# Optimization experiments

Measured on AMD Instinct MI355X. Metric: run time of the kernel, lower is better.

## Reference

```python
import jax, jax.numpy as jnp
import numpy as np

EMBED_DIM = 1024
NUM_HEADS = 16
HEAD_DIM = EMBED_DIM // NUM_HEADS
B, T = 4, 2048


def setup_inputs() -> dict:
    key = jax.random.key(0)
    ks = jax.random.split(key, 5)
    s = 1.0 / np.sqrt(EMBED_DIM)
    x = jax.random.normal(ks[0], (B, T, EMBED_DIM), dtype=jnp.float32)
    attention_mask = jnp.ones((B, 1, 1, T), dtype=jnp.int32)
    # torch Linear weights: qkv (3E, E), out (E, E); store transposed for x @ W
    W_qkv = jax.random.uniform(ks[1], (EMBED_DIM, 3 * EMBED_DIM), jnp.float32, -s, s)
    b_qkv = jax.random.uniform(ks[2], (3 * EMBED_DIM,), jnp.float32, -s, s)
    W_out = jax.random.uniform(ks[3], (EMBED_DIM, EMBED_DIM), jnp.float32, -s, s)
    b_out = jax.random.uniform(ks[4], (EMBED_DIM,), jnp.float32, -s, s)
    return {"x": x, "attention_mask": attention_mask,
            "W_qkv": W_qkv, "b_qkv": b_qkv, "W_out": W_out, "b_out": b_out}


def reference(x, attention_mask, W_qkv, b_qkv, W_out, b_out):
    Bq, Tq, E = x.shape
    qkv = x @ W_qkv + b_qkv                              # [B,T,3E]
    qkv = qkv.reshape(Bq, Tq, 3, NUM_HEADS, HEAD_DIM)
    qkv = jnp.transpose(qkv, (2, 0, 3, 1, 4))            # [3,B,H,T,d]
    q, k, v = qkv[0], qkv[1], qkv[2]
    scores = jnp.einsum('bhqd,bhkd->bhqk', q, k) / jnp.sqrt(
        jnp.asarray(HEAD_DIM, x.dtype))                  # [B,H,T,T]
    scores = jnp.where(attention_mask == 0, jnp.asarray(-jnp.inf, x.dtype), scores)
    attn = jax.nn.softmax(scores, axis=-1)
    ctx = jnp.einsum('bhqk,bhkd->bhqd', attn, v)         # [B,H,T,d]
    ctx = jnp.transpose(ctx, (0, 2, 1, 3)).reshape(Bq, Tq, E)
    return ctx @ W_out + b_out
```

## Files before the change

kernel.cpp:

```cpp
#include <hip/hip_runtime.h>
#include <hip/hip_bf16.h>
#include <stdint.h>


typedef __attribute__((ext_vector_type(8))) short short8;
typedef __attribute__((ext_vector_type(4))) float f32x4;
typedef __attribute__((ext_vector_type(16))) float f32x16;
typedef __attribute__((ext_vector_type(4))) unsigned short ushort4_t;
typedef __attribute__((ext_vector_type(8))) unsigned short ushort8_t;

#define SEQ 2048
#define EDIM 1024
#define QSCALE 0.18033688011112042f

__device__ __forceinline__ unsigned short f2bf(float x) {
  union { float f; uint32_t u; } v; v.f = x;
  uint32_t r = v.u + 0x7fffu + ((v.u >> 16) & 1u);
  return (unsigned short)(r >> 16);
}

__device__ __forceinline__ uint32_t cvtpk(float lo, float hi) {
  uint32_t r;
  asm("v_cvt_pk_bf16_f32 %0, %1, %2" : "=v"(r) : "v"(lo), "v"(hi));
  return r;
}

__device__ __forceinline__ float exp2_raw(float x) {
  float r;
  asm("v_exp_f32 %0, %1" : "=v"(r) : "v"(x));
  return r;
}

__device__ __forceinline__ void gload_lds16(const void* g, void* l) {
  typedef __attribute__((address_space(1))) const unsigned int gu32;
  typedef __attribute__((address_space(3))) unsigned int lu32;
  __builtin_amdgcn_global_load_lds((gu32*)g, (lu32*)l, 16, 0, 0);
}

__global__ void k_prep(const float* __restrict__ x,
                       unsigned short* __restrict__ xb,
                       const float* __restrict__ Wq,
                       unsigned short* __restrict__ wqt,
                       const float* __restrict__ Wo,
                       unsigned short* __restrict__ wot) {
  __shared__ float tile[32][33];
  const int id = blockIdx.x;
  if (id < 4096) {
    const int i = id * 256 + threadIdx.x;
    const float4* p = ((const float4*)x) + (size_t)i * 2;
    float4 a = p[0], b = p[1];
    ushort8_t v;
    v[0] = f2bf(a.x); v[1] = f2bf(a.y); v[2] = f2bf(a.z); v[3] = f2bf(a.w);
    v[4] = f2bf(b.x); v[5] = f2bf(b.y); v[6] = f2bf(b.z); v[7] = f2bf(b.w);
    ((ushort8_t*)xb)[i] = v;
    return;
  }
  const float* W;
  unsigned short* Wt;
  int N, bx, by;
  if (id < 7168) { W = Wq; Wt = wqt; N = 3072; bx = (id - 4096) % 96; by = (id - 4096) / 96; }
  else           { W = Wo; Wt = wot; N = 1024; bx = (id - 7168) % 32; by = (id - 7168) / 32; }
  const int K = 1024;
  const int c0 = bx * 32, r0 = by * 32;
  const int tx = threadIdx.x & 31, ty = threadIdx.x >> 5;
#pragma unroll
  for (int i = 0; i < 4; ++i) {
    int r = ty + i * 8;
    tile[r][tx] = W[(size_t)(r0 + r) * N + c0 + tx];
  }
  __syncthreads();
#pragma unroll
  for (int i = 0; i < 4; ++i) {
    int r = ty + i * 8;
    Wt[(size_t)(c0 + r) * K + r0 + tx] = f2bf(tile[tx][r]);
  }
}

template <int EPI, int NBX>
__global__ __launch_bounds__(256, 2) void k_gemm(
    const unsigned short* __restrict__ A, const unsigned short* __restrict__ Bt,
    const float* __restrict__ bias, unsigned short* __restrict__ Qo,
    unsigned short* __restrict__ Ko, unsigned short* __restrict__ VTo,
    float* __restrict__ Out) {
  __shared__ unsigned short As[2][128 * 32];
  __shared__ unsigned short Bs[2][128 * 32];
  const int tid = threadIdx.x;
  const int lane = tid & 63, wid = tid >> 6;
  const int wr = wid >> 1, wc = wid & 1;
  const int g = lane >> 4, r = lane & 15;
  const int lid = blockIdx.y * NBX + blockIdx.x;
  const int total = NBX * gridDim.y;
  const int id = (lid & 7) * (total >> 3) + (lid >> 3);
  const int m0 = (id / NBX) * 128, n0 = (id % NBX) * 128;

  const int row0 = tid >> 2, sl0 = tid & 3;
  const unsigned short* a0 = A + (size_t)(m0 + row0) * 1024 + sl0 * 8;
  const unsigned short* a1 = A + (size_t)(m0 + 64 + row0) * 1024 + sl0 * 8;
  const unsigned short* b0 = Bt + (size_t)(n0 + row0) * 1024 + sl0 * 8;
  const unsigned short* b1 = Bt + (size_t)(n0 + 64 + row0) * 1024 + sl0 * 8;
  char* adst = (char*)As[0] + wid * 64 * 16;
  char* bdst = (char*)Bs[0] + wid * 64 * 16;

  auto STAGE = [&](int buf) {
    const int bo = buf * 8192;
    gload_lds16(a0, adst + bo);        a0 += 32;
    gload_lds16(a1, adst + bo + 4096); a1 += 32;
    gload_lds16(b0, bdst + bo);        b0 += 32;
    gload_lds16(b1, bdst + bo + 4096); b1 += 32;
  };

  f32x4 zero4 = {0.f, 0.f, 0.f, 0.f};
  f32x4 acc[4][4];
#pragma unroll
  for (int mi = 0; mi < 4; ++mi)
#pragma unroll
    for (int ni = 0; ni < 4; ++ni) acc[mi][ni] = zero4;

  STAGE(0);
  asm volatile("s_waitcnt vmcnt(0)" ::: "memory");
  __builtin_amdgcn_s_barrier();

  for (int t = 0; t < 32; ++t) {
    const int cur = t & 1;
    if (t < 31) STAGE(cur ^ 1);
    short8 af[4], bf[4];
#pragma unroll
    for (int mi = 0; mi < 4; ++mi)
      af[mi] = *(const short8*)&As[cur][(wr * 64 + mi * 16 + r) * 32 + g * 8];
#pragma unroll
    for (int ni = 0; ni < 4; ++ni)
      bf[ni] = *(const short8*)&Bs[cur][(wc * 64 + ni * 16 + r) * 32 + g * 8];
#pragma unroll
    for (int mi = 0; mi < 4; ++mi)
#pragma unroll
      for (int ni = 0; ni < 4; ++ni)
        acc[mi][ni] = __builtin_amdgcn_mfma_f32_16x16x32_bf16(
            af[mi], bf[ni], acc[mi][ni], 0, 0, 0);
    asm volatile("s_waitcnt vmcnt(0)" ::: "memory");
    __builtin_amdgcn_s_barrier();
  }

#pragma unroll
  for (int mi = 0; mi < 4; ++mi) {
#pragma unroll
    for (int ni = 0; ni < 4; ++ni) {
      const int n = n0 + wc * 64 + ni * 16 + r;
      const float bv = bias[n];
      const int mbase = m0 + wr * 64 + mi * 16 + g * 4;
      if (EPI == 0) {
        const int sec = n >> 10, e = n & 1023, h = e >> 6, dd = e & 63;
        const int b = mbase >> 11, t = mbase & 2047;
        if (sec == 2) {
          ushort4_t pk;
#pragma unroll
          for (int j = 0; j < 4; ++j) pk[j] = f2bf(acc[mi][ni][j] + bv);
          *(ushort4_t*)&VTo[(((size_t)b * 16 + h) * 64 + dd) * 2048 + t] = pk;
        } else {
          unsigned short* dst = (sec == 0) ? Qo : Ko;
          const float scl = (sec == 0) ? QSCALE : 1.0f;
#pragma unroll
          for (int j = 0; j < 4; ++j)
            dst[(((size_t)b * 16 + h) * 2048 + t + j) * 64 + dd] =
                f2bf((acc[mi][ni][j] + bv) * scl);
        }
      } else {
#pragma unroll
        for (int j = 0; j < 4; ++j)
          Out[(size_t)(mbase + j) * 1024 + n] = acc[mi][ni][j] + bv;
      }
    }
  }
}

__global__ __launch_bounds__(512, 4) void k_attn(
    const unsigned short* __restrict__ Qg, const unsigned short* __restrict__ Kg,
    const unsigned short* __restrict__ VTg, const int* __restrict__ maskp,
    unsigned short* __restrict__ ctx) {
  __shared__ unsigned short Ks[2][64 * 64];
  __shared__ unsigned short Vs[2][64 * 64];
  const int tid = threadIdx.x, lane = tid & 63, wid = tid >> 6;
  const int q = lane & 31, hi = lane >> 5;
  const int id = blockIdx.x;
  const int slot = id >> 3;
  const int bh = (id & 7) * 8 + (slot >> 3);
  const int b = bh >> 4, h = bh & 15;
  const int q0 = (slot & 7) * 256 + wid * 32;
  const int qr = q0 + q;

  const unsigned short* Qb = Qg + (size_t)bh * SEQ * 64;
  const unsigned short* Kb = Kg + (size_t)bh * SEQ * 64;
  const unsigned short* Vb = VTg + (size_t)bh * 64 * SEQ;
  const int* mb = maskp + b * SEQ;

  const int r0_ = tid >> 3, sl0_ = (tid & 7) ^ (r0_ & 7);
  const unsigned short* kp0 = Kb + r0_ * 64 + sl0_ * 8;
  const unsigned short* vp0 = Vb + (size_t)r0_ * SEQ + sl0_ * 8;
  char* kbase = (char*)Ks[0] + wid * 1024;
  char* vbase = (char*)Vs[0] + wid * 1024;

  auto STAGE = [&](int buf) {
    const int bo = buf * 8192;
    gload_lds16(kp0, kbase + bo);
    gload_lds16(vp0, vbase + bo);
    kp0 += 64 * 64;
    vp0 += 64;
  };

  short8 qf[4];
#pragma unroll
  for (int ds = 0; ds < 4; ++ds)
    qf[ds] = *(const short8*)&Qb[(size_t)qr * 64 + ds * 16 + hi * 8];

  short8 onesf;
#pragma unroll
  for (int j = 0; j < 8; ++j) onesf[j] = (short)0x3F80;

  f32x16 z16 = {0.f,0.f,0.f,0.f,0.f,0.f,0.f,0.f,0.f,0.f,0.f,0.f,0.f,0.f,0.f,0.f};
  f32x16 o0 = z16, o1 = z16;
  f32x16 osum = z16;
  const int kb4 = hi * 4;

  STAGE(0);
  const int* mptr = mb + lane;
  int mv = mptr[0];
  mptr += 64;

  for (int t = 0; t < 32; ++t) {
    const int cur = t & 1;
    __syncthreads();
    int mvn = 1;
    if (t < 31) {
      STAGE(cur ^ 1);
      mvn = mptr[0];
      mptr += 64;
    }
    const unsigned long long bits = __ballot(mv != 0);
    mv = mvn;

    const char* KsB = (const char*)Ks[cur];
    const char* VsB = (const char*)Vs[cur];
    f32x16 c0 = z16, c1 = z16;
    __builtin_amdgcn_s_setprio(1);
#pragma unroll
    for (int ds = 0; ds < 4; ++ds) {
      const int sl = ds * 2 + hi;
      short8 ka0 = *(const short8*)(KsB + q * 128 + ((sl ^ (q & 7)) * 16));
      short8 ka1 = *(const short8*)(KsB + (32 + q) * 128 + ((sl ^ (q & 7)) * 16));
      c0 = __builtin_amdgcn_mfma_f32_32x32x16_bf16(ka0, qf[ds], c0, 0, 0, 0);
      c1 = __builtin_amdgcn_mfma_f32_32x32x16_bf16(ka1, qf[ds], c1, 0, 0, 0);
    }
    __builtin_amdgcn_s_setprio(0);

#pragma unroll
    for (int i = 0; i < 16; ++i) {
      c0[i] = exp2_raw(c0[i]);
      c1[i] = exp2_raw(c1[i]);
    }
    if (bits != ~0ull) {
#pragma unroll
      for (int i = 0; i < 16; ++i) {
        const int k0 = (i & 3) + 8 * (i >> 2) + kb4;
        if (!((bits >> k0) & 1)) c0[i] = 0.f;
        if (!((bits >> (k0 + 32)) & 1)) c1[i] = 0.f;
      }
    }

    short8 pf[4];
#pragma unroll
    for (int sub = 0; sub < 2; ++sub) {
      uint32_t w[8];
#pragma unroll
      for (int j = 0; j < 8; ++j)
        w[j] = sub ? cvtpk(c1[2 * j], c1[2 * j + 1])
                   : cvtpk(c0[2 * j], c0[2 * j + 1]);
      asm("v_permlane32_swap_b32 %0, %1" : "+v"(w[0]), "+v"(w[2]));
      asm("v_permlane32_swap_b32 %0, %1" : "+v"(w[1]), "+v"(w[3]));
      asm("v_permlane32_swap_b32 %0, %1" : "+v"(w[4]), "+v"(w[6]));
      asm("v_permlane32_swap_b32 %0, %1" : "+v"(w[5]), "+v"(w[7]));
      union { uint32_t u[4]; short8 s; } ua, ub;
      ua.u[0] = w[0]; ua.u[1] = w[1]; ua.u[2] = w[2]; ua.u[3] = w[3];
      ub.u[0] = w[4]; ub.u[1] = w[5]; ub.u[2] = w[6]; ub.u[3] = w[7];
      pf[sub * 2] = ua.s;
      pf[sub * 2 + 1] = ub.s;
    }

    __builtin_amdgcn_s_setprio(1);
#pragma unroll
    for (int ks = 0; ks < 4; ++ks) {
      const int sl = ks * 2 + hi;
      short8 va0 = *(const short8*)(VsB + q * 128 + ((sl ^ (q & 7)) * 16));
      short8 va1 = *(const short8*)(VsB + (32 + q) * 128 + ((sl ^ (q & 7)) * 16));
      o0 = __builtin_amdgcn_mfma_f32_32x32x16_bf16(va0, pf[ks], o0, 0, 0, 0);
      o1 = __builtin_amdgcn_mfma_f32_32x32x16_bf16(va1, pf[ks], o1, 0, 0, 0);
      osum = __builtin_amdgcn_mfma_f32_32x32x16_bf16(onesf, pf[ks], osum,
                                                     0, 0, 0);
    }
    __builtin_amdgcn_s_setprio(0);
  }

  const float inv = 1.f / osum[0];
#pragma unroll
  for (int ns = 0; ns < 2; ++ns) {
#pragma unroll
    for (int g_ = 0; g_ < 4; ++g_) {
      ushort4_t v4;
#pragma unroll
      for (int e = 0; e < 4; ++e) {
        const float val = (ns ? o1[g_ * 4 + e] : o0[g_ * 4 + e]) * inv;
        v4[e] = f2bf(val);
      }
      *(ushort4_t*)&ctx[((size_t)b * SEQ + qr) * 1024 + h * 64 + ns * 32 +
                        g_ * 8 + hi * 4] = v4;
    }
  }
}

extern "C" void kernel_launch(void* const* d_in, const int* in_sizes, int n_in,
                              void* d_out, int out_size, void* d_ws,
                              size_t ws_size, hipStream_t stream) {
  const float* x = (const float*)d_in[0];
  const int* mask = (const int*)d_in[1];
  const float* Wqkv = (const float*)d_in[2];
  const float* bqkv = (const float*)d_in[3];
  const float* Wout = (const float*)d_in[4];
  const float* bout = (const float*)d_in[5];
  float* out = (float*)d_out;

  unsigned short* ws = (unsigned short*)d_ws;
  unsigned short* xb = ws;
  unsigned short* wqt = ws + 8388608;
  unsigned short* wot = ws + 11534336;
  unsigned short* Q = ws + 12582912;
  unsigned short* K = ws + 20971520;
  unsigned short* VT = ws + 29360128;
  unsigned short* ctx = xb;

  k_prep<<<8192, 256, 0, stream>>>(x, xb, Wqkv, wqt, Wout, wot);
  k_gemm<0, 24><<<dim3(24, 64), 256, 0, stream>>>(xb, wqt, bqkv, Q, K, VT,
                                                  nullptr);
  k_attn<<<512, 512, 0, stream>>>(Q, K, VT, mask, ctx);
  k_gemm<1, 8><<<dim3(8, 64), 256, 0, stream>>>(ctx, wot, bout, nullptr,
                                                nullptr, nullptr, out);
}
```

Baseline: 198.2 us.

## Double the K-step per barrier in GEMM and attention, compute row sums in VALU

Both the projection GEMM and the attention kernel now stage two K/V (or A/B) sub-tiles per pipeline stage, which halves the number of barriers and loop iterations and issues more loads in flight per wait. The attention kernel also drops the extra ones-matrix MFMA that produced the softmax denominator and instead sums the exponentiated scores with VALU adds plus a cross-half shuffle. LDS use per block doubles, which may reduce occupancy (attention declares 4 blocks of 512 threads per CU) and puts more pressure on registers.

```diff
diff --git a/kernel.cpp b/kernel.cpp
--- a/kernel.cpp
+++ b/kernel.cpp
@@ -82,8 +82,8 @@
     const float* __restrict__ bias, unsigned short* __restrict__ Qo,
     unsigned short* __restrict__ Ko, unsigned short* __restrict__ VTo,
     float* __restrict__ Out) {
-  __shared__ unsigned short As[2][128 * 32];
-  __shared__ unsigned short Bs[2][128 * 32];
+  __shared__ unsigned short As[2][2][128 * 32];
+  __shared__ unsigned short Bs[2][2][128 * 32];
   const int tid = threadIdx.x;
   const int lane = tid & 63, wid = tid >> 6;
   const int wr = wid >> 1, wc = wid & 1;
@@ -98,15 +98,20 @@
   const unsigned short* a1 = A + (size_t)(m0 + 64 + row0) * 1024 + sl0 * 8;
   const unsigned short* b0 = Bt + (size_t)(n0 + row0) * 1024 + sl0 * 8;
   const unsigned short* b1 = Bt + (size_t)(n0 + 64 + row0) * 1024 + sl0 * 8;
-  char* adst = (char*)As[0] + wid * 64 * 16;
-  char* bdst = (char*)Bs[0] + wid * 64 * 16;
+  char* adst = (char*)As + wid * 64 * 16;
+  char* bdst = (char*)Bs + wid * 64 * 16;
 
   auto STAGE = [&](int buf) {
-    const int bo = buf * 8192;
-    gload_lds16(a0, adst + bo);        a0 += 32;
-    gload_lds16(a1, adst + bo + 4096); a1 += 32;
-    gload_lds16(b0, bdst + bo);        b0 += 32;
-    gload_lds16(b1, bdst + bo + 4096); b1 += 32;
+    const int bo = buf * 16384;
+    gload_lds16(a0,      adst + bo);
+    gload_lds16(a1,      adst + bo + 4096);
+    gload_lds16(a0 + 32, adst + bo + 8192);
+    gload_lds16(a1 + 32, adst + bo + 8192 + 4096);
+    gload_lds16(b0,      bdst + bo);
+    gload_lds16(b1,      bdst + bo + 4096);
+    gload_lds16(b0 + 32, bdst + bo + 8192);
+    gload_lds16(b1 + 32, bdst + bo + 8192 + 4096);
+    a0 += 64; a1 += 64; b0 += 64; b1 += 64;
   };
 
   f32x4 zero4 = {0.f, 0.f, 0.f, 0.f};
@@ -120,22 +125,25 @@
   asm volatile("s_waitcnt vmcnt(0)" ::: "memory");
   __builtin_amdgcn_s_barrier();
 
-  for (int t = 0; t < 32; ++t) {
+  for (int t = 0; t < 16; ++t) {
     const int cur = t & 1;
-    if (t < 31) STAGE(cur ^ 1);
-    short8 af[4], bf[4];
-#pragma unroll
-    for (int mi = 0; mi < 4; ++mi)
-      af[mi] = *(const short8*)&As[cur][(wr * 64 + mi * 16 + r) * 32 + g * 8];
-#pragma unroll
-    for (int ni = 0; ni < 4; ++ni)
-      bf[ni] = *(const short8*)&Bs[cur][(wc * 64 + ni * 16 + r) * 32 + g * 8];
-#pragma unroll
-    for (int mi = 0; mi < 4; ++mi)
+    if (t < 15) STAGE(cur ^ 1);
+#pragma unroll
+    for (int sub = 0; sub < 2; ++sub) {
+      short8 af[4], bf[4];
+#pragma unroll
+      for (int mi = 0; mi < 4; ++mi)
+        af[mi] = *(const short8*)&As[cur][sub][(wr * 64 + mi * 16 + r) * 32 + g * 8];
 #pragma unroll
       for (int ni = 0; ni < 4; ++ni)
-        acc[mi][ni] = __builtin_amdgcn_mfma_f32_16x16x32_bf16(
-            af[mi], bf[ni], acc[mi][ni], 0, 0, 0);
+        bf[ni] = *(const short8*)&Bs[cur][sub][(wc * 64 + ni * 16 + r) * 32 + g * 8];
+#pragma unroll
+      for (int mi = 0; mi < 4; ++mi)
+#pragma unroll
+        for (int ni = 0; ni < 4; ++ni)
+          acc[mi][ni] = __builtin_amdgcn_mfma_f32_16x16x32_bf16(
+              af[mi], bf[ni], acc[mi][ni], 0, 0, 0);
+    }
     asm volatile("s_waitcnt vmcnt(0)" ::: "memory");
     __builtin_amdgcn_s_barrier();
   }
@@ -176,8 +184,8 @@
     const unsigned short* __restrict__ Qg, const unsigned short* __restrict__ Kg,
     const unsigned short* __restrict__ VTg, const int* __restrict__ maskp,
     unsigned short* __restrict__ ctx) {
-  __shared__ unsigned short Ks[2][64 * 64];
-  __shared__ unsigned short Vs[2][64 * 64];
+  __shared__ unsigned short Ks[2][2][64 * 64];
+  __shared__ unsigned short Vs[2][2][64 * 64];
   const int tid = threadIdx.x, lane = tid & 63, wid = tid >> 6;
   const int q = lane & 31, hi = lane >> 5;
   const int id = blockIdx.x;
@@ -195,15 +203,17 @@
   const int r0_ = tid >> 3, sl0_ = (tid & 7) ^ (r0_ & 7);
   const unsigned short* kp0 = Kb + r0_ * 64 + sl0_ * 8;
   const unsigned short* vp0 = Vb + (size_t)r0_ * SEQ + sl0_ * 8;
-  char* kbase = (char*)Ks[0] + wid * 1024;
-  char* vbase = (char*)Vs[0] + wid * 1024;
+  char* kbase = (char*)Ks + wid * 1024;
+  char* vbase = (char*)Vs + wid * 1024;
 
   auto STAGE = [&](int buf) {
-    const int bo = buf * 8192;
-    gload_lds16(kp0, kbase + bo);
-    gload_lds16(vp0, vbase + bo);
-    kp0 += 64 * 64;
-    vp0 += 64;
+    const int bo = buf * 16384;
+    gload_lds16(kp0,        kbase + bo);
+    gload_lds16(kp0 + 4096, kbase + bo + 8192);
+    gload_lds16(vp0,        vbase + bo);
+    gload_lds16(vp0 + 64,   vbase + bo + 8192);
+    kp0 += 8192;
+    vp0 += 128;
   };
 
   short8 qf[4];
@@ -211,94 +221,108 @@
   for (int ds = 0; ds < 4; ++ds)
     qf[ds] = *(const short8*)&Qb[(size_t)qr * 64 + ds * 16 + hi * 8];
 
-  short8 onesf;
-#pragma unroll
-  for (int j = 0; j < 8; ++j) onesf[j] = (short)0x3F80;
-
   f32x16 z16 = {0.f,0.f,0.f,0.f,0.f,0.f,0.f,0.f,0.f,0.f,0.f,0.f,0.f,0.f,0.f,0.f};
   f32x16 o0 = z16, o1 = z16;
-  f32x16 osum = z16;
+  float lrun = 0.f;
   const int kb4 = hi * 4;
 
   STAGE(0);
   const int* mptr = mb + lane;
-  int mv = mptr[0];
-  mptr += 64;
-
-  for (int t = 0; t < 32; ++t) {
+  int mv0 = mptr[0], mv1 = mptr[64];
+  mptr += 128;
+
+  for (int t = 0; t < 16; ++t) {
     const int cur = t & 1;
     __syncthreads();
-    int mvn = 1;
-    if (t < 31) {
+    int mn0 = 1, mn1 = 1;
+    if (t < 15) {
       STAGE(cur ^ 1);
-      mvn = mptr[0];
-      mptr += 64;
-    }
-    const unsigned long long bits = __ballot(mv != 0);
-    mv = mvn;
-
-    const char* KsB = (const char*)Ks[cur];
-    const char* VsB = (const char*)Vs[cur];
-    f32x16 c0 = z16, c1 = z16;
-    __builtin_amdgcn_s_setprio(1);
-#pragma unroll
-    for (int ds = 0; ds < 4; ++ds) {
-      const int sl = ds * 2 + hi;
-      short8 ka0 = *(const short8*)(KsB + q * 128 + ((sl ^ (q & 7)) * 16));
-      short8 ka1 = *(const short8*)(KsB + (32 + q) * 128 + ((sl ^ (q & 7)) * 16));
-      c0 = __builtin_amdgcn_mfma_f32_32x32x16_bf16(ka0, qf[ds], c0, 0, 0, 0);
-      c1 = __builtin_amdgcn_mfma_f32_32x32x16_bf16(ka1, qf[ds], c1, 0, 0, 0);
-    }
-    __builtin_amdgcn_s_setprio(0);
-
-#pragma unroll
-    for (int i = 0; i < 16; ++i) {
-      c0[i] = exp2_raw(c0[i]);
-      c1[i] = exp2_raw(c1[i]);
-    }
-    if (bits != ~0ull) {
+      mn0 = mptr[0]; mn1 = mptr[64];
+      mptr += 128;
+    }
+    const unsigned long long bits0 = __ballot(mv0 != 0);
+    const unsigned long long bits1 = __ballot(mv1 != 0);
+    mv0 = mn0; mv1 = mn1;
+
+#pragma unroll
+    for (int sub = 0; sub < 2; ++sub) {
+      const char* KsB = (const char*)Ks + cur * 16384 + sub * 8192;
+      const char* VsB = (const char*)Vs + cur * 16384 + sub * 8192;
+      const unsigned long long bits = sub ? bits1 : bits0;
+
+      f32x16 c0 = z16, c1 = z16;
+      __builtin_amdgcn_s_setprio(1);
+#pragma unroll
+      for (int ds = 0; ds < 4; ++ds) {
+        const int sl = ds * 2 + hi;
+        short8 ka0 = *(const short8*)(KsB + q * 128 + ((sl ^ (q & 7)) * 16));
+        short8 ka1 = *(const short8*)(KsB + (32 + q) * 128 + ((sl ^ (q & 7)) * 16));
+        c0 = __builtin_amdgcn_mfma_f32_32x32x16_bf16(ka0, qf[ds], c0, 0, 0, 0);
+        c1 = __builtin_amdgcn_mfma_f32_32x32x16_bf16(ka1, qf[ds], c1, 0, 0, 0);
+      }
+      __builtin_amdgcn_s_setprio(0);
+
 #pragma unroll
       for (int i = 0; i < 16; ++i) {
-        const int k0 = (i & 3) + 8 * (i >> 2) + kb4;
-        if (!((bits >> k0) & 1)) c0[i] = 0.f;
-        if (!((bits >> (k0 + 32)) & 1)) c1[i] = 0.f;
-      }
-    }
-
-    short8 pf[4];
-#pragma unroll
-    for (int sub = 0; sub < 2; ++sub) {
-      uint32_t w[8];
-#pragma unroll
-      for (int j = 0; j < 8; ++j)
-        w[j] = sub ? cvtpk(c1[2 * j], c1[2 * j + 1])
-                   : cvtpk(c0[2 * j], c0[2 * j + 1]);
-      asm("v_permlane32_swap_b32 %0, %1" : "+v"(w[0]), "+v"(w[2]));
-      asm("v_permlane32_swap_b32 %0, %1" : "+v"(w[1]), "+v"(w[3]));
-      asm("v_permlane32_swap_b32 %0, %1" : "+v"(w[4]), "+v"(w[6]));
-      asm("v_permlane32_swap_b32 %0, %1" : "+v"(w[5]), "+v"(w[7]));
-      union { uint32_t u[4]; short8 s; } ua, ub;
-      ua.u[0] = w[0]; ua.u[1] = w[1]; ua.u[2] = w[2]; ua.u[3] = w[3];
-      ub.u[0] = w[4]; ub.u[1] = w[5]; ub.u[2] = w[6]; ub.u[3] = w[7];
-      pf[sub * 2] = ua.s;
-      pf[sub * 2 + 1] = ub.s;
-    }
-
-    __builtin_amdgcn_s_setprio(1);
-#pragma unroll
-    for (int ks = 0; ks < 4; ++ks) {
-      const int sl = ks * 2 + hi;
-      short8 va0 = *(const short8*)(VsB + q * 128 + ((sl ^ (q & 7)) * 16));
-      short8 va1 = *(const short8*)(VsB + (32 + q) * 128 + ((sl ^ (q & 7)) * 16));
-      o0 = __builtin_amdgcn_mfma_f32_32x32x16_bf16(va0, pf[ks], o0, 0, 0, 0);
-      o1 = __builtin_amdgcn_mfma_f32_32x32x16_bf16(va1, pf[ks], o1, 0, 0, 0);
-      osum = __builtin_amdgcn_mfma_f32_32x32x16_bf16(onesf, pf[ks], osum,
-                                                     0, 0, 0);
-    }
-    __builtin_amdgcn_s_setprio(0);
-  }
-
-  const float inv = 1.f / osum[0];
+        c0[i] = exp2_raw(c0[i]);
+        c1[i] = exp2_raw(c1[i]);
+      }
+      if (bits != ~0ull) {
+#pragma unroll
+        for (int i = 0; i < 16; ++i) {
+          const int k0 = (i & 3) + 8 * (i >> 2) + kb4;
+          if (!((bits >> k0) & 1)) c0[i] = 0.f;
+          if (!((bits >> (k0 + 32)) & 1)) c1[i] = 0.f;
+        }
+      }
+
+      {
+        float s0 = 0.f, s1 = 0.f, s2 = 0.f, s3 = 0.f;
+#pragma unroll
+        for (int i = 0; i < 16; i += 4) {
+          s0 += c0[i]     + c1[i];
+          s1 += c0[i + 1] + c1[i + 1];
+          s2 += c0[i + 2] + c1[i + 2];
+          s3 += c0[i + 3] + c1[i + 3];
+        }
+        float ts = (s0 + s1) + (s2 + s3);
+        ts += __shfl_xor(ts, 32);
+        lrun += ts;
+      }
+
+      short8 pf[4];
+#pragma unroll
+      for (int s_ = 0; s_ < 2; ++s_) {
+        uint32_t w[8];
+#pragma unroll
+        for (int j = 0; j < 8; ++j)
+          w[j] = s_ ? cvtpk(c1[2 * j], c1[2 * j + 1])
+                    : cvtpk(c0[2 * j], c0[2 * j + 1]);
+        asm("v_permlane32_swap_b32 %0, %1" : "+v"(w[0]), "+v"(w[2]));
+        asm("v_permlane32_swap_b32 %0, %1" : "+v"(w[1]), "+v"(w[3]));
+        asm("v_permlane32_swap_b32 %0, %1" : "+v"(w[4]), "+v"(w[6]));
+        asm("v_permlane32_swap_b32 %0, %1" : "+v"(w[5]), "+v"(w[7]));
+        union { uint32_t u[4]; short8 s; } ua, ub;
+        ua.u[0] = w[0]; ua.u[1] = w[1]; ua.u[2] = w[2]; ua.u[3] = w[3];
+        ub.u[0] = w[4]; ub.u[1] = w[5]; ub.u[2] = w[6]; ub.u[3] = w[7];
+        pf[s_ * 2] = ua.s;
+        pf[s_ * 2 + 1] = ub.s;
+      }
+
+      __builtin_amdgcn_s_setprio(1);
+#pragma unroll
+      for (int ks = 0; ks < 4; ++ks) {
+        const int sl = ks * 2 + hi;
+        short8 va0 = *(const short8*)(VsB + q * 128 + ((sl ^ (q & 7)) * 16));
+        short8 va1 = *(const short8*)(VsB + (32 + q) * 128 + ((sl ^ (q & 7)) * 16));
+        o0 = __builtin_amdgcn_mfma_f32_32x32x16_bf16(va0, pf[ks], o0, 0, 0, 0);
+        o1 = __builtin_amdgcn_mfma_f32_32x32x16_bf16(va1, pf[ks], o1, 0, 0, 0);
+      }
+      __builtin_amdgcn_s_setprio(0);
+    }
+  }
+
+  const float inv = 1.f / lrun;
 #pragma unroll
   for (int ns = 0; ns < 2; ++ns) {
 #pragma unroll
```

Result: no change. 197.3 us (-0.4%).
